# Performance work log

Measured on AMD Instinct MI355X. Metric: run time of the kernel, lower is better.

The kernel has to match this reference:

```python
import jax, jax.numpy as jnp
import numpy as np

HEAD = 8
EMB = 512
D_K = EMB // HEAD


def setup_inputs() -> dict:
    key = jax.random.key(0)
    ks = jax.random.split(key, 12)
    B, S = 2, 2048
    scale = 1.0 / np.sqrt(EMB)
    inp = {
        "query": jax.random.normal(ks[0], (B, S, EMB), jnp.float32),
        "key": jax.random.normal(ks[1], (B, S, EMB), jnp.float32),
        "value": jax.random.normal(ks[2], (B, S, EMB), jnp.float32),
        # subsequentMask(size): lower-triangular causal mask, shape [1, S, S]
        "mask": jnp.tril(jnp.ones((1, S, S), jnp.int32)),
        "Wq": jax.random.normal(ks[3], (EMB, EMB), jnp.float32) * scale,
        "bq": jnp.zeros((EMB,), jnp.float32),
        "Wk": jax.random.normal(ks[4], (EMB, EMB), jnp.float32) * scale,
        "bk": jnp.zeros((EMB,), jnp.float32),
        "Wv": jax.random.normal(ks[5], (EMB, EMB), jnp.float32) * scale,
        "bv": jnp.zeros((EMB,), jnp.float32),
        "Wo": jax.random.normal(ks[6], (EMB, EMB), jnp.float32) * scale,
        "bo": jnp.zeros((EMB,), jnp.float32),
    }
    return inp


def _split_heads(x, B):
    # [B, S, E] -> [B, H, S, d_k]
    return x.reshape(B, -1, HEAD, D_K).transpose(0, 2, 1, 3)


def reference(query, key, value, mask, Wq, bq, Wk, bk, Wv, bv, Wo, bo):
    B, S, _ = query.shape
    # linear projections (x @ W^T + b, torch nn.Linear convention)
    q = _split_heads(query @ Wq.T + bq, B)
    k = _split_heads(key @ Wk.T + bk, B)
    v = _split_heads(value @ Wv.T + bv, B)
    # scaled dot-product attention; scores [B, H, S, S]
    scores = jnp.einsum('bhqd,bhkd->bhqk', q, k) / jnp.sqrt(jnp.float32(D_K))
    # mask [1,S,S] -> unsqueeze(0) -> [1,1,S,S]; masked_fill(mask==0, -1e9)
    m = mask[None, ...]  # [1, 1, S, S]
    scores = jnp.where(m == 0, jnp.float32(-1e9), scores)
    p_attn = jax.nn.softmax(scores, axis=-1)
    # dropout is identity at inference (deterministic reference)
    x = jnp.einsum('bhqk,bhkd->bhqd', p_attn, v)
    x = x.transpose(0, 2, 1, 3).reshape(B, S, EMB)
    return x @ Wo.T + bo
```

## Files before the change

kernel.cpp:

```cpp
#include <hip/hip_runtime.h>
#include <hip/hip_bf16.h>


#define SEQ 2048
#define EMB 512
#define NH  8
#define DKD 64

typedef __bf16 bf16x8 __attribute__((ext_vector_type(8)));
typedef float  f32x4  __attribute__((ext_vector_type(4)));

__device__ __forceinline__ ushort f2bf(float f) {
  unsigned x = __float_as_uint(f);
  return (ushort)((x + 0x7fffu + ((x >> 16) & 1u)) >> 16);
}
__device__ __forceinline__ unsigned pkbf(float a, float b) {
  __hip_bfloat162 h = __float22bfloat162_rn(make_float2(a, b));
  unsigned u;
  __builtin_memcpy(&u, &h, 4);
  return u;
}

__device__ __forceinline__ void cp16(const ushort* g, ushort* l) {
  __builtin_amdgcn_global_load_lds(
      (const __attribute__((address_space(1))) void*)g,
      (__attribute__((address_space(3))) void*)l, 16, 0, 0);
}

__global__ __launch_bounds__(256) void cvt7(
    const float* s0, const float* s1, const float* s2, const float* s3,
    const float* s4, const float* s5, const float* s6,
    ushort* d0, ushort* d1, ushort* d2, ushort* d3,
    ushort* d4, ushort* d5, ushort* d6) {
  const float* src; ushort* dst; int n;
  switch (blockIdx.y) {
    case 0: src = s0; dst = d0; n = 2 * SEQ * EMB; break;
    case 1: src = s1; dst = d1; n = 2 * SEQ * EMB; break;
    case 2: src = s2; dst = d2; n = 2 * SEQ * EMB; break;
    case 3: src = s3; dst = d3; n = EMB * EMB;     break;
    case 4: src = s4; dst = d4; n = EMB * EMB;     break;
    case 5: src = s5; dst = d5; n = EMB * EMB;     break;
    default: src = s6; dst = d6; n = EMB * EMB;    break;
  }
  int i = (blockIdx.x * 256 + threadIdx.x) * 8;
  if (i >= n) return;
  float4 a = *reinterpret_cast<const float4*>(src + i);
  float4 b = *reinterpret_cast<const float4*>(src + i + 4);
  uint4 t = make_uint4(pkbf(a.x, a.y), pkbf(a.z, a.w),
                       pkbf(b.x, b.y), pkbf(b.z, b.w));
  *reinterpret_cast<uint4*>(dst + i) = t;
}

__device__ __forceinline__ void gemm_body(const ushort* __restrict__ X,
                                          const ushort* __restrict__ W,
                                          const float* __restrict__ bias,
                                          void* __restrict__ C,
                                          int mode, bool of32, float oscale,
                                          ushort* sA, ushort* sB) {
  const int N = EMB, K = EMB;
  const int tid = threadIdx.x;
  const int w = tid >> 6, lane = tid & 63, r16 = lane & 15, g = lane >> 4;
  const int nT = N / 64;
  const int m0 = (blockIdx.x / nT) * 128;
  const int n0 = (blockIdx.x % nT) * 64;
  const int wm = w * 32;

  f32x4 acc[2][4] = {};

  auto stage = [&](int buf, int k0) {
#pragma unroll
    for (int i = 0; i < 2; ++i) {
      const int s = i * 256 + w * 64 + lane;
      const int row = s >> 2;
      const int col = (s & 3) ^ ((row >> 1) & 3);
      cp16(X + (size_t)(m0 + row) * K + k0 + col * 8, sA + buf * 4096 + s * 8);
    }
    {
      const int s = w * 64 + lane;
      const int row = s >> 2;
      const int col = (s & 3) ^ ((row >> 1) & 3);
      cp16(W + (size_t)(n0 + row) * K + k0 + col * 8, sB + buf * 2048 + s * 8);
    }
  };

  stage(0, 0);
  const int NIT = K / 32;
  for (int it = 0; it < NIT; ++it) {
    const int cur = it & 1;
    __syncthreads();
    if (it + 1 < NIT) stage(cur ^ 1, (it + 1) * 32);

    const ushort* bA = sA + cur * 4096;
    const ushort* bB = sB + cur * 2048;
    bf16x8 af[2], bfr[4];
#pragma unroll
    for (int f = 0; f < 2; ++f) {
      const int row = wm + f * 16 + r16;
      af[f] = *reinterpret_cast<const bf16x8*>(bA + row * 32 + ((g ^ ((row >> 1) & 3)) << 3));
    }
#pragma unroll
    for (int t = 0; t < 4; ++t) {
      const int row = t * 16 + r16;
      bfr[t] = *reinterpret_cast<const bf16x8*>(bB + row * 32 + ((g ^ ((row >> 1) & 3)) << 3));
    }
#pragma unroll
    for (int f = 0; f < 2; ++f)
#pragma unroll
      for (int t = 0; t < 4; ++t)
        acc[f][t] = __builtin_amdgcn_mfma_f32_16x16x32_bf16(af[f], bfr[t], acc[f][t], 0, 0, 0);
  }

#pragma unroll
  for (int t = 0; t < 4; ++t) {
    const int n = n0 + t * 16 + r16;
    const float bv = bias[n];
#pragma unroll
    for (int f = 0; f < 2; ++f) {
#pragma unroll
      for (int r = 0; r < 4; ++r) {
        const int m = m0 + wm + f * 16 + g * 4 + r;
        const float v = (acc[f][t][r] + bv) * oscale;
        size_t addr;
        if (mode == 0) {
          addr = (size_t)m * N + n;
        } else {
          const int b = m >> 11, s = m & (SEQ - 1);
          const int h = n >> 6, dk = n & (DKD - 1);
          addr = (mode == 1) ? (((size_t)(b * NH + h) * SEQ + s) * DKD + dk)
                             : (((size_t)(b * NH + h) * DKD + dk) * SEQ + s);
        }
        if (of32) ((float*)C)[addr] = v;
        else      ((ushort*)C)[addr] = f2bf(v);
      }
    }
  }
}

__global__ __launch_bounds__(256) void proj_qkv(
    const ushort* Xq, const ushort* Xk, const ushort* Xv,
    const ushort* Wq, const ushort* Wk, const ushort* Wv,
    const float* bq, const float* bk, const float* bv,
    ushort* Qo, ushort* Ko, ushort* Vo) {
  __shared__ __align__(16) ushort sA[2 * 128 * 32];
  __shared__ __align__(16) ushort sB[2 * 64 * 32];
  const int z = blockIdx.z;
  const ushort* X = (z == 0) ? Xq : (z == 1) ? Xk : Xv;
  const ushort* W = (z == 0) ? Wq : (z == 1) ? Wk : Wv;
  const float* bias = (z == 0) ? bq : (z == 1) ? bk : bv;
  ushort* C = (z == 0) ? Qo : (z == 1) ? Ko : Vo;
  gemm_body(X, W, bias, C, (z == 2) ? 2 : 1, false,
            (z == 0) ? 0.18033688011112042f : 1.0f, sA, sB);
}

__global__ __launch_bounds__(256) void out_proj(const ushort* X, const ushort* W,
                                                const float* bias, float* C) {
  __shared__ __align__(16) ushort sA[2 * 128 * 32];
  __shared__ __align__(16) ushort sB[2 * 64 * 32];
  gemm_body(X, W, bias, C, 0, true, 1.0f, sA, sB);
}

__global__ __launch_bounds__(256) void flash_attn(const ushort* __restrict__ Q,
                                                  const ushort* __restrict__ Kb,
                                                  const ushort* __restrict__ Vt,
                                                  float* __restrict__ O0,
                                                  float* __restrict__ O1,
                                                  float* __restrict__ O2,
                                                  float* __restrict__ P0,
                                                  float* __restrict__ P1,
                                                  float* __restrict__ P2) {
  __shared__ __align__(16) ushort sK[64 * 64];
  __shared__ __align__(16) ushort sV[64 * 64];
  __shared__ __align__(16) ushort sP[4][16 * 64];

  const int tid = threadIdx.x, w = tid >> 6, lane = tid & 63;
  const int r16 = lane & 15, g = lane >> 4;
  const int sp = blockIdx.x % 3;
  const int c  = blockIdx.x / 3;
  const int bh = c & 15;
  const int qb = c >> 4;
  const int tiles = qb + 1;
  const int kt0 = (tiles * sp) / 3;
  const int kt1 = (tiles * (sp + 1)) / 3;

  const int q0 = qb * 64 + w * 16;
  const int q  = q0 + r16;

  const ushort* qp = Q + ((size_t)bh * SEQ + q0 + r16) * DKD + g * 8;
  const bf16x8 qf0 = *reinterpret_cast<const bf16x8*>(qp);
  const bf16x8 qf1 = *reinterpret_cast<const bf16x8*>(qp + 32);

  f32x4 oacc[4] = {};
  float psum = 0.f;

  const ushort* kbase = Kb + (size_t)bh * SEQ * DKD;
  const ushort* vbase = Vt + (size_t)bh * DKD * SEQ;

  auto stageKV = [&](int kb) {
#pragma unroll
    for (int i = 0; i < 2; ++i) {
      const int s = i * 256 + w * 64 + lane;
      const int row = s >> 3;
      const int col = (s & 7) ^ (row & 7);
      cp16(kbase + (size_t)(kb + row) * DKD + col * 8, &sK[(size_t)(i * 256 + w * 64) * 8]);
      cp16(vbase + (size_t)row * SEQ + kb + col * 8,   &sV[(size_t)(i * 256 + w * 64) * 8]);
    }
  };

  for (int kt = kt0; kt < kt1; ++kt) {
    const int kb = kt * 64;
    __syncthreads();
    stageKV(kb);
    __syncthreads();

    f32x4 sc[4] = {};
#pragma unroll
    for (int t = 0; t < 4; ++t) {
      const int row = t * 16 + r16;
      const bf16x8 a0 = *reinterpret_cast<const bf16x8*>(&sK[row * 64 + (((0 + g) ^ (row & 7)) << 3)]);
      const bf16x8 a1 = *reinterpret_cast<const bf16x8*>(&sK[row * 64 + (((4 + g) ^ (row & 7)) << 3)]);
      sc[t] = __builtin_amdgcn_mfma_f32_16x16x32_bf16(a0, qf0, sc[t], 0, 0, 0);
      sc[t] = __builtin_amdgcn_mfma_f32_16x16x32_bf16(a1, qf1, sc[t], 0, 0, 0);
    }

    const bool diag = (kb + 63) > q0;
    float p[16];
#pragma unroll
    for (int t = 0; t < 4; ++t)
#pragma unroll
      for (int r = 0; r < 4; ++r) {
        float e = __builtin_amdgcn_exp2f(sc[t][r]);
        if (diag && (kb + t * 16 + g * 4 + r) > q) e = 0.f;
        p[t * 4 + r] = e;
      }
    float s0 = (p[0] + p[1]) + (p[2] + p[3]);
    float s1 = (p[4] + p[5]) + (p[6] + p[7]);
    float s2 = (p[8] + p[9]) + (p[10] + p[11]);
    float s3 = (p[12] + p[13]) + (p[14] + p[15]);
    psum += (s0 + s1) + (s2 + s3);

#pragma unroll
    for (int t = 0; t < 4; ++t) {
      const unsigned lo = pkbf(p[t * 4],     p[t * 4 + 1]);
      const unsigned hi = pkbf(p[t * 4 + 2], p[t * 4 + 3]);
      const int key0 = t * 16 + g * 4;
      const int slot = (key0 >> 3) ^ (r16 & 7);
      *reinterpret_cast<uint2*>(&sP[w][r16 * 64 + slot * 8 + (key0 & 7)]) = make_uint2(lo, hi);
    }
    __asm__ volatile("s_waitcnt lgkmcnt(0)" ::: "memory");

    const bf16x8 pf0 = *reinterpret_cast<const bf16x8*>(&sP[w][r16 * 64 + (((0 + g) ^ (r16 & 7)) << 3)]);
    const bf16x8 pf1 = *reinterpret_cast<const bf16x8*>(&sP[w][r16 * 64 + (((4 + g) ^ (r16 & 7)) << 3)]);
#pragma unroll
    for (int t = 0; t < 4; ++t) {
      const int row = t * 16 + r16;
      const bf16x8 b0 = *reinterpret_cast<const bf16x8*>(&sV[row * 64 + (((0 + g) ^ (row & 7)) << 3)]);
      const bf16x8 b1 = *reinterpret_cast<const bf16x8*>(&sV[row * 64 + (((4 + g) ^ (row & 7)) << 3)]);
      oacc[t] = __builtin_amdgcn_mfma_f32_16x16x32_bf16(pf0, b0, oacc[t], 0, 0, 0);
      oacc[t] = __builtin_amdgcn_mfma_f32_16x16x32_bf16(pf1, b1, oacc[t], 0, 0, 0);
    }
  }

  psum += __shfl_xor(psum, 16);
  psum += __shfl_xor(psum, 32);
  float* Pc = (sp == 0) ? P0 : (sp == 1) ? P1 : P2;
  float* Oc = (sp == 0) ? O0 : (sp == 1) ? O1 : O2;
  if (g == 0) Pc[(size_t)bh * SEQ + q0 + r16] = psum;
#pragma unroll
  for (int r = 0; r < 4; ++r) {
    const int mq = q0 + g * 4 + r;
#pragma unroll
    for (int t = 0; t < 4; ++t)
      Oc[((size_t)bh * SEQ + mq) * DKD + t * 16 + r16] = oacc[t][r];
  }
}

__global__ __launch_bounds__(256) void attn_norm(const float* __restrict__ O0,
                                                 const float* __restrict__ O1,
                                                 const float* __restrict__ O2,
                                                 const float* __restrict__ P0,
                                                 const float* __restrict__ P1,
                                                 const float* __restrict__ P2,
                                                 ushort* __restrict__ Ab) {
  const int idx = blockIdx.x * 256 + threadIdx.x;
  const int d0 = (idx & 7) * 8;
  const int s  = (idx >> 3) & (SEQ - 1);
  const int bh = idx >> 14;
  const size_t o = ((size_t)bh * SEQ + s) * DKD + d0;
  const float4 a0 = *reinterpret_cast<const float4*>(O0 + o);
  const float4 a1 = *reinterpret_cast<const float4*>(O0 + o + 4);
  const float4 b0 = *reinterpret_cast<const float4*>(O1 + o);
  const float4 b1 = *reinterpret_cast<const float4*>(O1 + o + 4);
  const float4 c0 = *reinterpret_cast<const float4*>(O2 + o);
  const float4 c1 = *reinterpret_cast<const float4*>(O2 + o + 4);
  const size_t ps = (size_t)bh * SEQ + s;
  const float inv = 1.0f / (P0[ps] + P1[ps] + P2[ps]);
  uint4 t = make_uint4(
      pkbf((a0.x + b0.x + c0.x) * inv, (a0.y + b0.y + c0.y) * inv),
      pkbf((a0.z + b0.z + c0.z) * inv, (a0.w + b0.w + c0.w) * inv),
      pkbf((a1.x + b1.x + c1.x) * inv, (a1.y + b1.y + c1.y) * inv),
      pkbf((a1.z + b1.z + c1.z) * inv, (a1.w + b1.w + c1.w) * inv));
  const int b = bh >> 3, h = bh & 7;
  *reinterpret_cast<uint4*>(Ab + ((size_t)b * SEQ + s) * EMB + h * DKD + d0) = t;
}

extern "C" void kernel_launch(void* const* d_in, const int* in_sizes, int n_in,
                              void* d_out, int out_size, void* d_ws, size_t ws_size,
                              hipStream_t stream) {
  const float* q_in = (const float*)d_in[0];
  const float* k_in = (const float*)d_in[1];
  const float* v_in = (const float*)d_in[2];
  const float* Wq = (const float*)d_in[4];
  const float* bq = (const float*)d_in[5];
  const float* Wk = (const float*)d_in[6];
  const float* bk = (const float*)d_in[7];
  const float* Wv = (const float*)d_in[8];
  const float* bv = (const float*)d_in[9];
  const float* Wo = (const float*)d_in[10];
  const float* bo = (const float*)d_in[11];
  float* out = (float*)d_out;
  ushort* ws = (ushort*)d_ws;

  const size_t NX = (size_t)2 * SEQ * EMB;
  const size_t NW = (size_t)EMB * EMB;
  const size_t NO = (size_t)2 * NH * SEQ * DKD;
  ushort* Xq = ws;
  ushort* Xk = Xq + NX;
  ushort* Xv = Xk + NX;
  ushort* WqB = Xv + NX;
  ushort* WkB = WqB + NW;
  ushort* WvB = WkB + NW;
  ushort* WoB = WvB + NW;
  ushort* Qb  = WoB + NW;
  ushort* Kbf = Qb + NX;
  ushort* Vbf = Kbf + NX;
  ushort* Ab  = Vbf + NX;
  float*  O0  = (float*)(Ab + NX);
  float*  O1  = O0 + NO;
  float*  O2  = O1 + NO;
  float*  P0  = O2 + NO;
  float*  P1  = P0 + (size_t)2 * NH * SEQ;
  float*  P2  = P1 + (size_t)2 * NH * SEQ;

  dim3 blk(256);
  cvt7<<<dim3(1024, 7), blk, 0, stream>>>(q_in, k_in, v_in, Wq, Wk, Wv, Wo,
                                          Xq, Xk, Xv, WqB, WkB, WvB, WoB);
  proj_qkv<<<dim3((2 * SEQ / 128) * (EMB / 64), 1, 3), blk, 0, stream>>>(
      Xq, Xk, Xv, WqB, WkB, WvB, bq, bk, bv, Qb, Kbf, Vbf);
  flash_attn<<<dim3(512 * 3), blk, 0, stream>>>(Qb, Kbf, Vbf, O0, O1, O2, P0, P1, P2);
  attn_norm<<<dim3(1024), blk, 0, stream>>>(O0, O1, O2, P0, P1, P2, Ab);
  out_proj<<<dim3((2 * SEQ / 128) * (EMB / 64)), blk, 0, stream>>>(Ab, WoB, bo, out);
}
```

Baseline: 165.4 us.

## Store split-K partial outputs in fp16 and remap blocks for XCD locality

```diff
diff --git a/kernel.cpp b/kernel.cpp
--- a/kernel.cpp
+++ b/kernel.cpp
@@ -9,6 +9,7 @@
 
 typedef __bf16 bf16x8 __attribute__((ext_vector_type(8)));
 typedef float  f32x4  __attribute__((ext_vector_type(4)));
+typedef _Float16 f16x8 __attribute__((ext_vector_type(8)));
 
 __device__ __forceinline__ ushort f2bf(float f) {
   unsigned x = __float_as_uint(f);
@@ -55,14 +56,15 @@
                                           const ushort* __restrict__ W,
                                           const float* __restrict__ bias,
                                           void* __restrict__ C,
-                                          int mode, bool of32, float oscale,
+                                          int wg, int mode, bool of32,
+                                          float oscale,
                                           ushort* sA, ushort* sB) {
   const int N = EMB, K = EMB;
   const int tid = threadIdx.x;
   const int w = tid >> 6, lane = tid & 63, r16 = lane & 15, g = lane >> 4;
   const int nT = N / 64;
-  const int m0 = (blockIdx.x / nT) * 128;
-  const int n0 = (blockIdx.x % nT) * 64;
+  const int m0 = (wg / nT) * 128;
+  const int n0 = (wg % nT) * 64;
   const int wm = w * 32;
 
   f32x4 acc[2][4] = {};
@@ -148,7 +150,9 @@
   const ushort* W = (z == 0) ? Wq : (z == 1) ? Wk : Wv;
   const float* bias = (z == 0) ? bq : (z == 1) ? bk : bv;
   ushort* C = (z == 0) ? Qo : (z == 1) ? Ko : Vo;
-  gemm_body(X, W, bias, C, (z == 2) ? 2 : 1, false,
+  const int h = blockIdx.x;
+  const int wg = (h & 7) * 32 + (h >> 3);
+  gemm_body(X, W, bias, C, wg, (z == 2) ? 2 : 1, false,
             (z == 0) ? 0.18033688011112042f : 1.0f, sA, sB);
 }
 
@@ -156,15 +160,17 @@
                                                 const float* bias, float* C) {
   __shared__ __align__(16) ushort sA[2 * 128 * 32];
   __shared__ __align__(16) ushort sB[2 * 64 * 32];
-  gemm_body(X, W, bias, C, 0, true, 1.0f, sA, sB);
+  const int h = blockIdx.x;
+  const int wg = (h & 7) * 32 + (h >> 3);
+  gemm_body(X, W, bias, C, wg, 0, true, 1.0f, sA, sB);
 }
 
 __global__ __launch_bounds__(256) void flash_attn(const ushort* __restrict__ Q,
                                                   const ushort* __restrict__ Kb,
                                                   const ushort* __restrict__ Vt,
-                                                  float* __restrict__ O0,
-                                                  float* __restrict__ O1,
-                                                  float* __restrict__ O2,
+                                                  _Float16* __restrict__ O0,
+                                                  _Float16* __restrict__ O1,
+                                                  _Float16* __restrict__ O2,
                                                   float* __restrict__ P0,
                                                   float* __restrict__ P1,
                                                   float* __restrict__ P2) {
@@ -174,10 +180,12 @@
 
   const int tid = threadIdx.x, w = tid >> 6, lane = tid & 63;
   const int r16 = lane & 15, g = lane >> 4;
-  const int sp = blockIdx.x % 3;
-  const int c  = blockIdx.x / 3;
-  const int bh = c & 15;
-  const int qb = c >> 4;
+  const int hwid = blockIdx.x;
+  const int xcd = hwid & 7;
+  const int j   = hwid >> 3;
+  const int bh  = xcd * 2 + (j & 1);
+  const int qb  = 31 - ((j >> 1) & 31);
+  const int sp  = j >> 6;
   const int tiles = qb + 1;
   const int kt0 = (tiles * sp) / 3;
   const int kt1 = (tiles * (sp + 1)) / 3;
@@ -263,20 +271,20 @@
   psum += __shfl_xor(psum, 16);
   psum += __shfl_xor(psum, 32);
   float* Pc = (sp == 0) ? P0 : (sp == 1) ? P1 : P2;
-  float* Oc = (sp == 0) ? O0 : (sp == 1) ? O1 : O2;
+  _Float16* Oc = (sp == 0) ? O0 : (sp == 1) ? O1 : O2;
   if (g == 0) Pc[(size_t)bh * SEQ + q0 + r16] = psum;
 #pragma unroll
   for (int r = 0; r < 4; ++r) {
     const int mq = q0 + g * 4 + r;
 #pragma unroll
     for (int t = 0; t < 4; ++t)
-      Oc[((size_t)bh * SEQ + mq) * DKD + t * 16 + r16] = oacc[t][r];
-  }
-}
-
-__global__ __launch_bounds__(256) void attn_norm(const float* __restrict__ O0,
-                                                 const float* __restrict__ O1,
-                                                 const float* __restrict__ O2,
+      Oc[((size_t)bh * SEQ + mq) * DKD + t * 16 + r16] = (_Float16)oacc[t][r];
+  }
+}
+
+__global__ __launch_bounds__(256) void attn_norm(const _Float16* __restrict__ O0,
+                                                 const _Float16* __restrict__ O1,
+                                                 const _Float16* __restrict__ O2,
                                                  const float* __restrict__ P0,
                                                  const float* __restrict__ P1,
                                                  const float* __restrict__ P2,
@@ -286,21 +294,19 @@
   const int s  = (idx >> 3) & (SEQ - 1);
   const int bh = idx >> 14;
   const size_t o = ((size_t)bh * SEQ + s) * DKD + d0;
-  const float4 a0 = *reinterpret_cast<const float4*>(O0 + o);
-  const float4 a1 = *reinterpret_cast<const float4*>(O0 + o + 4);
-  const float4 b0 = *reinterpret_cast<const float4*>(O1 + o);
-  const float4 b1 = *reinterpret_cast<const float4*>(O1 + o + 4);
-  const float4 c0 = *reinterpret_cast<const float4*>(O2 + o);
-  const float4 c1 = *reinterpret_cast<const float4*>(O2 + o + 4);
+  const f16x8 a = *reinterpret_cast<const f16x8*>(O0 + o);
+  const f16x8 b = *reinterpret_cast<const f16x8*>(O1 + o);
+  const f16x8 c = *reinterpret_cast<const f16x8*>(O2 + o);
   const size_t ps = (size_t)bh * SEQ + s;
   const float inv = 1.0f / (P0[ps] + P1[ps] + P2[ps]);
-  uint4 t = make_uint4(
-      pkbf((a0.x + b0.x + c0.x) * inv, (a0.y + b0.y + c0.y) * inv),
-      pkbf((a0.z + b0.z + c0.z) * inv, (a0.w + b0.w + c0.w) * inv),
-      pkbf((a1.x + b1.x + c1.x) * inv, (a1.y + b1.y + c1.y) * inv),
-      pkbf((a1.z + b1.z + c1.z) * inv, (a1.w + b1.w + c1.w) * inv));
-  const int b = bh >> 3, h = bh & 7;
-  *reinterpret_cast<uint4*>(Ab + ((size_t)b * SEQ + s) * EMB + h * DKD + d0) = t;
+  float r[8];
+#pragma unroll
+  for (int i = 0; i < 8; ++i)
+    r[i] = ((float)a[i] + (float)b[i] + (float)c[i]) * inv;
+  uint4 t = make_uint4(pkbf(r[0], r[1]), pkbf(r[2], r[3]),
+                       pkbf(r[4], r[5]), pkbf(r[6], r[7]));
+  const int bb = bh >> 3, hh = bh & 7;
+  *reinterpret_cast<uint4*>(Ab + ((size_t)bb * SEQ + s) * EMB + hh * DKD + d0) = t;
 }
 
 extern "C" void kernel_launch(void* const* d_in, const int* in_sizes, int n_in,
@@ -334,10 +340,10 @@
   ushort* Kbf = Qb + NX;
   ushort* Vbf = Kbf + NX;
   ushort* Ab  = Vbf + NX;
-  float*  O0  = (float*)(Ab + NX);
-  float*  O1  = O0 + NO;
-  float*  O2  = O1 + NO;
-  float*  P0  = O2 + NO;
+  _Float16* O0 = (_Float16*)(Ab + NX);
+  _Float16* O1 = O0 + NO;
+  _Float16* O2 = O1 + NO;
+  float*  P0  = (float*)(O2 + NO);
   float*  P1  = P0 + (size_t)2 * NH * SEQ;
   float*  P2  = P1 + (size_t)2 * NH * SEQ;
 
```

After: 154.4 us. 1.07x faster.
